# Performance work log

Hardware: AMD Instinct MI355X
Metric: run time of the kernel (lower is better)

The kernel has to match this reference:

```python
import jax, jax.numpy as jnp
import numpy as np

N = 100000      # num_nodes
E = 800000      # num_edges (avg degree 8)
F_IN = 64
F_OUT = 64
H = 4           # num_heads
HOPS = 2        # num_hops
NEG_SLOPE = 0.2


def setup_inputs() -> dict:
    key = jax.random.key(0)
    ks = jax.random.split(key, 9)
    node_features = jax.random.normal(ks[0], (N, F_IN), jnp.float32)
    edge_index = jax.random.randint(ks[1], (2, E), 0, N, dtype=jnp.int64)
    s_in = 1.0 / np.sqrt(F_IN)
    s_out = 1.0 / np.sqrt(F_OUT)
    W_att = jax.random.normal(ks[2], (H, F_IN, F_OUT), jnp.float32) * s_in
    a_src = jax.random.normal(ks[3], (H, F_OUT), jnp.float32) * s_out
    a_dst = jax.random.normal(ks[4], (H, F_OUT), jnp.float32) * s_out
    W_g = jax.random.normal(ks[5], (F_IN, F_OUT), jnp.float32) * s_in
    b_g = jnp.zeros((F_OUT,), jnp.float32)
    W_w = jax.random.normal(ks[6], (2 * F_OUT, F_OUT), jnp.float32) * (1.0 / np.sqrt(2 * F_OUT))
    b_w = jnp.zeros((F_OUT,), jnp.float32)
    return {"node_features": node_features, "edge_index": edge_index,
            "W_att": W_att, "a_src": a_src, "a_dst": a_dst,
            "W_g": W_g, "b_g": b_g, "W_w": W_w, "b_w": b_w}


def _segment_softmax(scores, dst, num_segments):
    # scores: [E, H], softmax over edges sharing the same destination node
    m = jax.ops.segment_max(scores, dst, num_segments=num_segments)  # [N, H]
    m = jnp.where(jnp.isneginf(m), 0.0, m)
    ex = jnp.exp(scores - m[dst])                                    # [E, H]
    den = jax.ops.segment_sum(ex, dst, num_segments=num_segments)   # [N, H]
    return ex / jnp.maximum(den[dst], 1e-16)


def _multi_head_attention(x, src, dst, W_att, a_src, a_dst):
    h = jnp.einsum('ni,hio->nho', x, W_att)                          # [N, H, O]
    e = jnp.einsum('eho,ho->eh', h[src], a_src) \
        + jnp.einsum('eho,ho->eh', h[dst], a_dst)                    # [E, H]
    e = jax.nn.leaky_relu(e, NEG_SLOPE)
    alpha = _segment_softmax(e, dst, N)                              # [E, H]
    msg = alpha[:, :, None] * h[src]                                 # [E, H, O]
    out = jax.ops.segment_sum(msg, dst, num_segments=N)              # [N, H, O]
    return out.mean(axis=1)                                          # average heads -> [N, O]


def _gf(x, src, dst, num_hops):
    # multi-hop mean-neighbor aggregation
    ones = jnp.ones((src.shape[0],), x.dtype)
    deg = jax.ops.segment_sum(ones, dst, num_segments=N)             # [N]
    deg = jnp.maximum(deg, 1.0)[:, None]
    h = x
    for _ in range(num_hops):
        h = jax.ops.segment_sum(h[src], dst, num_segments=N) / deg
    return h


def reference(node_features, edge_index, W_att, a_src, a_dst, W_g, b_g, W_w, b_w):
    src, dst = edge_index[0], edge_index[1]
    local = _multi_head_attention(node_features, src, dst, W_att, a_src, a_dst)  # [N, O]
    glob = _gf(node_features, src, dst, HOPS)                                    # [N, F_IN]
    glob = glob @ W_g + b_g                                                      # [N, O]
    # dropout is identity in eval-mode reference
    cat = jnp.concatenate([local, glob], axis=-1)                                # [N, 2O]
    return cat @ W_w + b_w                                                       # [N, O]
```

## Files before the change

kernel.cpp:

```cpp
#include <hip/hip_runtime.h>
#include <math.h>

#define NN 100000
#define EE 800000
#define FDIM 64
#define NH 4
#define NEG 0.2f

#define SCAN_BLK 1024
#define SCAN_NBLK 98
#define HIST_BLK 3125
#define KH_BLK   6250

#define OFF_XB     0ull
#define OFF_HOP1   12800000ull
#define OFF_HOP2   25600000ull
#define OFF_SSRC   38400000ull
#define OFF_SDST   40000000ull
#define OFF_DEGC   41600000ull
#define OFF_ROWS   42000000ull
#define OFF_CURS   42400000ull
#define OFF_DEGF   42800000ull
#define OFF_PART   43200000ull
#define OFF_CSRS   43201024ull
#define OFF_WCAT   46401024ull
#define OFF_BCOMB  46417408ull
#define OFF_WT     46417664ull
#define OFF_WAS    46450432ull
#define OFF_WAD    46451456ull
#define WS_NEEDED  46452480ull

typedef __attribute__((ext_vector_type(8))) short bf16x8;
typedef __attribute__((ext_vector_type(4))) float f32x4;

__device__ __forceinline__ float bflo(unsigned int u) { return __uint_as_float(u << 16); }
__device__ __forceinline__ float bfhi(unsigned int u) { return __uint_as_float(u & 0xffff0000u); }
__device__ __forceinline__ unsigned short f2bf(float f) {
    unsigned int u = __float_as_uint(f);
    unsigned int r = u + 0x7fffu + ((u >> 16) & 1u);
    return (unsigned short)(r >> 16);
}
__device__ __forceinline__ float lrelu(float x) { return x > 0.f ? x : NEG * x; }

__global__ __launch_bounds__(256) void k_pre(
    const float* __restrict__ Watt, const float* __restrict__ asrc,
    const float* __restrict__ adst, const float* __restrict__ Wg,
    const float* __restrict__ bg, const float* __restrict__ Ww,
    const float* __restrict__ bw, const int* __restrict__ dst,
    unsigned short* __restrict__ Wt, float* __restrict__ waS, float* __restrict__ waD,
    unsigned short* __restrict__ Wcat, float* __restrict__ bc, int* __restrict__ degc)
{
    __shared__ float WcS[64][4];
    const int b = blockIdx.x, t = threadIdx.x;
    if (b < 8) {
        for (int idx = b * 2048 + t; idx < (b + 1) * 2048; idx += 256) {
            const int h = idx >> 12, o = (idx >> 6) & 63, k = idx & 63;
            Wt[idx] = f2bf(Watt[h * 4096 + k * 64 + o]);
        }
        if (b == 0) {
            const int h = t >> 6, i = t & 63;
            float aS = 0.f, aD = 0.f;
            for (int o = 0; o < 64; o++) {
                const float w = Watt[h * 4096 + i * 64 + o];
                aS += w * asrc[h * 64 + o];
                aD += w * adst[h * 64 + o];
            }
            waS[t] = aS;
            waD[t] = aD;
        }
    } else if (b < 24) {
        const int c0 = (b - 8) * 4;
        {
            const int r = t >> 2, ci = t & 3;
            float a = 0.f;
            for (int m = 0; m < 64; m++) a += Wg[r * 64 + m] * Ww[(64 + m) * 64 + c0 + ci];
            WcS[r][ci] = a;
        }
        if (b == 8 && t < 64) {
            float a = bw[t];
            for (int m = 0; m < 64; m++) a += bg[m] * Ww[(64 + m) * 64 + t];
            bc[t] = a;
        }
        __syncthreads();
        for (int idx = t; idx < 512; idx += 256) {
            const int ci = idx >> 7, k = idx & 127;
            const int c = c0 + ci;
            const float v = (k < 64) ? Ww[k * 64 + c] : WcS[k - 64][ci];
            Wcat[c * 128 + k] = f2bf(v);
        }
    } else {
        const int e = (b - 24) * 256 + t;
        if (e < EE) atomicAdd(&degc[dst[e]], 1);
    }
}

__global__ __launch_bounds__(1024) void k_scan_a(const int* __restrict__ degc, int* __restrict__ part) {
    __shared__ int sh[1024];
    int t = threadIdx.x;
    int i = blockIdx.x * SCAN_BLK + t;
    sh[t] = (i < NN) ? degc[i] : 0;
    __syncthreads();
    for (int off = 512; off > 0; off >>= 1) {
        if (t < off) sh[t] += sh[t + off];
        __syncthreads();
    }
    if (t == 0) part[blockIdx.x] = sh[0];
}

__global__ __launch_bounds__(128) void k_scan_b(int* part) {
    __shared__ int sh[128];
    int t = threadIdx.x;
    int v = (t < SCAN_NBLK) ? part[t] : 0;
    sh[t] = v;
    __syncthreads();
    for (int off = 1; off < 128; off <<= 1) {
        int tmp = (t >= off) ? sh[t - off] : 0;
        __syncthreads();
        sh[t] += tmp;
        __syncthreads();
    }
    if (t < SCAN_NBLK) part[t] = sh[t] - v;
}

__global__ __launch_bounds__(1024) void k_scan_c(
    const int* __restrict__ degc, const int* __restrict__ part,
    int* __restrict__ rows, int* __restrict__ curs, float* __restrict__ degf)
{
    __shared__ int sh[1024];
    int t = threadIdx.x;
    int i = blockIdx.x * SCAN_BLK + t;
    int v = (i < NN) ? degc[i] : 0;
    sh[t] = v;
    __syncthreads();
    for (int off = 1; off < 1024; off <<= 1) {
        int tmp = (t >= off) ? sh[t - off] : 0;
        __syncthreads();
        sh[t] += tmp;
        __syncthreads();
    }
    int excl = sh[t] - v + part[blockIdx.x];
    if (i < NN) {
        rows[i] = excl;
        curs[i] = excl;
        degf[i] = (float)max(v, 1);
    }
}

__global__ __launch_bounds__(256) void k_mid(
    const int* __restrict__ srcp, const int* __restrict__ dstp,
    int* __restrict__ curs, int* __restrict__ csrs,
    const float* __restrict__ x, const float* __restrict__ waS,
    const float* __restrict__ waD, unsigned short* __restrict__ xb,
    float* __restrict__ ssrc, float* __restrict__ sdst)
{
    __shared__ float xs[16 * 64];
    __shared__ unsigned short xsb[16 * 64];
    __shared__ float wl[2 * 256];
    const int t = threadIdx.x;
    if (blockIdx.x < HIST_BLK) {
        const int e = blockIdx.x * 256 + t;
        if (e < EE) {
            const int d = dstp[e];
            const int pos = atomicAdd(&curs[d], 1);
            csrs[pos] = srcp[e];
        }
        return;
    }
    const int n0 = (blockIdx.x - HIST_BLK) * 16;
    {
        const int r = t >> 4, c4 = (t & 15) * 4;
        const float4 v = *(const float4*)&x[(size_t)(n0 + r) * 64 + c4];
        *(float4*)&xs[r * 64 + c4] = v;
        uint2 p;
        p.x = (unsigned int)f2bf(v.x) | ((unsigned int)f2bf(v.y) << 16);
        p.y = (unsigned int)f2bf(v.z) | ((unsigned int)f2bf(v.w) << 16);
        *(uint2*)&xsb[r * 64 + c4] = p;
        wl[t] = waS[t];
        wl[256 + t] = waD[t];
    }
    __syncthreads();
    if (t < 128) {
        const int r = t >> 3, c8 = (t & 7) * 8;
        const uint4 v = *(const uint4*)&xsb[r * 64 + c8];
        *(uint4*)&xb[(size_t)(n0 + r) * 64 + c8] = v;
    }
    {
        const int nl = t >> 4, hh = (t >> 2) & 3, q = t & 3;
        const float* xr = &xs[nl * 64 + q * 16];
        const float* wS = &wl[hh * 64 + q * 16];
        const float* wD = &wl[256 + hh * 64 + q * 16];
        float pS = 0.f, pD = 0.f;
#pragma unroll
        for (int i = 0; i < 16; i++) { pS += xr[i] * wS[i]; pD += xr[i] * wD[i]; }
        pS += __shfl_xor(pS, 1); pS += __shfl_xor(pS, 2);
        pD += __shfl_xor(pD, 1); pD += __shfl_xor(pD, 2);
        if (q == 0) {
            ssrc[(n0 + nl) * 4 + hh] = pS;
            sdst[(n0 + nl) * 4 + hh] = pD;
        }
    }
}

__global__ __launch_bounds__(256) void k_attn2(
    const unsigned short* __restrict__ xb, const unsigned short* __restrict__ Wt,
    const float* __restrict__ ssrc, const float* __restrict__ sdst,
    const int* __restrict__ rows, const int* __restrict__ degc,
    const float* __restrict__ degf, const int* __restrict__ csrs,
    unsigned short* __restrict__ hop1b, char* __restrict__ outb)
{
    __shared__ unsigned short ysh[4][16][72];
    __shared__ float dsh[4][16][66];
    const int t = threadIdx.x;
    const int w = t >> 6, lane = t & 63;
    const int nl = (lane >> 4) & 3;
    const int e  = (lane >> 3) & 1;
    const int cl = lane & 7;
    const int n = blockIdx.x * 16 + w * 4 + nl;
    const int start = rows[n], cnt = degc[n];
    int cmax = cnt;
    cmax = max(cmax, __shfl_xor(cmax, 16));
    cmax = max(cmax, __shfl_xor(cmax, 32));
    const float4 sd = *(const float4*)&sdst[n * 4];
    float y0[8], y1[8], y2[8], y3[8], hp[8];
#pragma unroll
    for (int c = 0; c < 8; c++) { y0[c]=0.f; y1[c]=0.f; y2[c]=0.f; y3[c]=0.f; hp[c]=0.f; }
    float d0 = 0.f, d1 = 0.f, d2 = 0.f, d3 = 0.f;
    for (int base = 0; base < cmax; base += 2) {
        const int j = base + e;
        const bool valid = j < cnt;
        const int idx = min(start + j, EE - 1);
        const int s = csrs[idx];
        const float4 ss = *(const float4*)&ssrc[s * 4];
        float e0 = __expf(lrelu(ss.x + sd.x));
        float e1 = __expf(lrelu(ss.y + sd.y));
        float e2 = __expf(lrelu(ss.z + sd.z));
        float e3 = __expf(lrelu(ss.w + sd.w));
        float hw = 1.f;
        if (!valid) { e0 = 0.f; e1 = 0.f; e2 = 0.f; e3 = 0.f; hw = 0.f; }
        d0 += e0; d1 += e1; d2 += e2; d3 += e3;
        const uint4 u = *(const uint4*)&xb[(size_t)s * 64 + cl * 8];
        float xv[8];
        xv[0] = bflo(u.x); xv[1] = bfhi(u.x);
        xv[2] = bflo(u.y); xv[3] = bfhi(u.y);
        xv[4] = bflo(u.z); xv[5] = bfhi(u.z);
        xv[6] = bflo(u.w); xv[7] = bfhi(u.w);
#pragma unroll
        for (int c = 0; c < 8; c++) {
            y0[c] += e0 * xv[c];
            y1[c] += e1 * xv[c];
            y2[c] += e2 * xv[c];
            y3[c] += e3 * xv[c];
            hp[c] += hw * xv[c];
        }
    }
#pragma unroll
    for (int c = 0; c < 8; c++) {
        y0[c] += __shfl_xor(y0[c], 8);
        y1[c] += __shfl_xor(y1[c], 8);
        y2[c] += __shfl_xor(y2[c], 8);
        y3[c] += __shfl_xor(y3[c], 8);
        hp[c] += __shfl_xor(hp[c], 8);
    }
    d0 += __shfl_xor(d0, 8);
    d1 += __shfl_xor(d1, 8);
    d2 += __shfl_xor(d2, 8);
    d3 += __shfl_xor(d3, 8);
    if (e == 0) {
        const float i0 = (cnt > 0) ? 1.f / d0 : 0.f;
        const float i1 = (cnt > 0) ? 1.f / d1 : 0.f;
        const float i2 = (cnt > 0) ? 1.f / d2 : 0.f;
        const float i3 = (cnt > 0) ? 1.f / d3 : 0.f;
        const int nloc = w * 4 + nl;
        uint4 p;
        p.x = (unsigned int)f2bf(y0[0]*i0) | ((unsigned int)f2bf(y0[1]*i0) << 16);
        p.y = (unsigned int)f2bf(y0[2]*i0) | ((unsigned int)f2bf(y0[3]*i0) << 16);
        p.z = (unsigned int)f2bf(y0[4]*i0) | ((unsigned int)f2bf(y0[5]*i0) << 16);
        p.w = (unsigned int)f2bf(y0[6]*i0) | ((unsigned int)f2bf(y0[7]*i0) << 16);
        *(uint4*)&ysh[0][nloc][cl * 8] = p;
        p.x = (unsigned int)f2bf(y1[0]*i1) | ((unsigned int)f2bf(y1[1]*i1) << 16);
        p.y = (unsigned int)f2bf(y1[2]*i1) | ((unsigned int)f2bf(y1[3]*i1) << 16);
        p.z = (unsigned int)f2bf(y1[4]*i1) | ((unsigned int)f2bf(y1[5]*i1) << 16);
        p.w = (unsigned int)f2bf(y1[6]*i1) | ((unsigned int)f2bf(y1[7]*i1) << 16);
        *(uint4*)&ysh[1][nloc][cl * 8] = p;
        p.x = (unsigned int)f2bf(y2[0]*i2) | ((unsigned int)f2bf(y2[1]*i2) << 16);
        p.y = (unsigned int)f2bf(y2[2]*i2) | ((unsigned int)f2bf(y2[3]*i2) << 16);
        p.z = (unsigned int)f2bf(y2[4]*i2) | ((unsigned int)f2bf(y2[5]*i2) << 16);
        p.w = (unsigned int)f2bf(y2[6]*i2) | ((unsigned int)f2bf(y2[7]*i2) << 16);
        *(uint4*)&ysh[2][nloc][cl * 8] = p;
        p.x = (unsigned int)f2bf(y3[0]*i3) | ((unsigned int)f2bf(y3[1]*i3) << 16);
        p.y = (unsigned int)f2bf(y3[2]*i3) | ((unsigned int)f2bf(y3[3]*i3) << 16);
        p.z = (unsigned int)f2bf(y3[4]*i3) | ((unsigned int)f2bf(y3[5]*i3) << 16);
        p.w = (unsigned int)f2bf(y3[6]*i3) | ((unsigned int)f2bf(y3[7]*i3) << 16);
        *(uint4*)&ysh[3][nloc][cl * 8] = p;
        const float iv = 1.f / degf[n];
        p.x = (unsigned int)f2bf(hp[0]*iv) | ((unsigned int)f2bf(hp[1]*iv) << 16);
        p.y = (unsigned int)f2bf(hp[2]*iv) | ((unsigned int)f2bf(hp[3]*iv) << 16);
        p.z = (unsigned int)f2bf(hp[4]*iv) | ((unsigned int)f2bf(hp[5]*iv) << 16);
        p.w = (unsigned int)f2bf(hp[6]*iv) | ((unsigned int)f2bf(hp[7]*iv) << 16);
        *(uint4*)&hop1b[(size_t)n * 64 + cl * 8] = p;
    }
    __syncthreads();
    {
        const int m = lane & 15, quad = lane >> 4;
        const bf16x8 a0 = *(const bf16x8*)&ysh[w][m][quad * 8];
        const bf16x8 a1 = *(const bf16x8*)&ysh[w][m][32 + quad * 8];
        f32x4 acc[4] = {{0.f,0.f,0.f,0.f},{0.f,0.f,0.f,0.f},{0.f,0.f,0.f,0.f},{0.f,0.f,0.f,0.f}};
#pragma unroll
        for (int ot = 0; ot < 4; ot++) {
            const unsigned short* wp = Wt + w * 4096 + (ot * 16 + m) * 64 + quad * 8;
            const bf16x8 b0 = *(const bf16x8*)wp;
            const bf16x8 b1 = *(const bf16x8*)(wp + 32);
            acc[ot] = __builtin_amdgcn_mfma_f32_16x16x32_bf16(a0, b0, acc[ot], 0, 0, 0);
            acc[ot] = __builtin_amdgcn_mfma_f32_16x16x32_bf16(a1, b1, acc[ot], 0, 0, 0);
        }
#pragma unroll
        for (int ot = 0; ot < 4; ot++)
#pragma unroll
            for (int r = 0; r < 4; r++)
                dsh[w][quad * 4 + r][ot * 16 + m] = acc[ot][r];
    }
    __syncthreads();
    {
        const int n2 = t >> 4, c4 = (t & 15) * 4;
        float o0 = 0.25f * (dsh[0][n2][c4+0] + dsh[1][n2][c4+0] + dsh[2][n2][c4+0] + dsh[3][n2][c4+0]);
        float o1 = 0.25f * (dsh[0][n2][c4+1] + dsh[1][n2][c4+1] + dsh[2][n2][c4+1] + dsh[3][n2][c4+1]);
        float o2 = 0.25f * (dsh[0][n2][c4+2] + dsh[1][n2][c4+2] + dsh[2][n2][c4+2] + dsh[3][n2][c4+2]);
        float o3 = 0.25f * (dsh[0][n2][c4+3] + dsh[1][n2][c4+3] + dsh[2][n2][c4+3] + dsh[3][n2][c4+3]);
        uint2 p;
        p.x = (unsigned int)f2bf(o0) | ((unsigned int)f2bf(o1) << 16);
        p.y = (unsigned int)f2bf(o2) | ((unsigned int)f2bf(o3) << 16);
        *(uint2*)(outb + ((size_t)(blockIdx.x * 16 + n2)) * 256 + (t & 15) * 8) = p;
    }
}

__global__ __launch_bounds__(256) void k_hop(
    const unsigned short* __restrict__ xin, const int* __restrict__ rows,
    const int* __restrict__ degc, const float* __restrict__ degf,
    const int* __restrict__ csrs, unsigned short* __restrict__ out_b)
{
    const int lane = threadIdx.x & 63;
    const int n = blockIdx.x * 4 + (threadIdx.x >> 6);
    if (n >= NN) return;
    const int start = rows[n], cnt = degc[n];
    const int g = lane >> 3;
    const int c8 = (lane & 7) * 8;
    float a0=0.f,a1=0.f,a2=0.f,a3=0.f,a4=0.f,a5=0.f,a6=0.f,a7=0.f;
    for (int j = g; j < cnt; j += 8) {
        const int s = csrs[start + j];
        const uint4 u = *(const uint4*)&xin[(size_t)s * 64 + c8];
        a0 += bflo(u.x); a1 += bfhi(u.x);
        a2 += bflo(u.y); a3 += bfhi(u.y);
        a4 += bflo(u.z); a5 += bfhi(u.z);
        a6 += bflo(u.w); a7 += bfhi(u.w);
    }
#pragma unroll
    for (int off = 8; off < 64; off <<= 1) {
        a0 += __shfl_xor(a0, off); a1 += __shfl_xor(a1, off);
        a2 += __shfl_xor(a2, off); a3 += __shfl_xor(a3, off);
        a4 += __shfl_xor(a4, off); a5 += __shfl_xor(a5, off);
        a6 += __shfl_xor(a6, off); a7 += __shfl_xor(a7, off);
    }
    if (lane < 8) {
        const float inv = 1.f / degf[n];
        uint4 p;
        p.x = (unsigned int)f2bf(a0 * inv) | ((unsigned int)f2bf(a1 * inv) << 16);
        p.y = (unsigned int)f2bf(a2 * inv) | ((unsigned int)f2bf(a3 * inv) << 16);
        p.z = (unsigned int)f2bf(a4 * inv) | ((unsigned int)f2bf(a5 * inv) << 16);
        p.w = (unsigned int)f2bf(a6 * inv) | ((unsigned int)f2bf(a7 * inv) << 16);
        *(uint4*)&out_b[(size_t)n * 64 + c8] = p;
    }
}

__global__ __launch_bounds__(256) void k_final(
    const unsigned short* __restrict__ Wcat, const float* __restrict__ bc,
    const unsigned short* __restrict__ hop2b, float* __restrict__ outp)
{
    __shared__ float os[64 * 68];
    __shared__ float bcl[64];
    const int t = threadIdx.x;
    const int n0 = blockIdx.x * 64;
    if (t < 64) bcl[t] = bc[t];
    const int w = t >> 6, lane = t & 63, m = lane & 15, quad = lane >> 4;
    const int node = n0 + w * 16 + m;
    const int nld = min(node, NN - 1);
    const unsigned short* lrow = (const unsigned short*)((const char*)outp + (size_t)nld * 256);
    const unsigned short* grow = &hop2b[(size_t)nld * 64];
    const bf16x8 a0 = *(const bf16x8*)&lrow[quad * 8];
    const bf16x8 a1 = *(const bf16x8*)&lrow[32 + quad * 8];
    const bf16x8 a2 = *(const bf16x8*)&grow[quad * 8];
    const bf16x8 a3 = *(const bf16x8*)&grow[32 + quad * 8];
    f32x4 acc[4] = {{0.f,0.f,0.f,0.f},{0.f,0.f,0.f,0.f},{0.f,0.f,0.f,0.f},{0.f,0.f,0.f,0.f}};
#pragma unroll
    for (int ot = 0; ot < 4; ot++) {
        const unsigned short* wp = Wcat + (ot * 16 + m) * 128 + quad * 8;
        const bf16x8 b0 = *(const bf16x8*)wp;
        const bf16x8 b1 = *(const bf16x8*)(wp + 32);
        const bf16x8 b2 = *(const bf16x8*)(wp + 64);
        const bf16x8 b3 = *(const bf16x8*)(wp + 96);
        acc[ot] = __builtin_amdgcn_mfma_f32_16x16x32_bf16(a0, b0, acc[ot], 0, 0, 0);
        acc[ot] = __builtin_amdgcn_mfma_f32_16x16x32_bf16(a1, b1, acc[ot], 0, 0, 0);
        acc[ot] = __builtin_amdgcn_mfma_f32_16x16x32_bf16(a2, b2, acc[ot], 0, 0, 0);
        acc[ot] = __builtin_amdgcn_mfma_f32_16x16x32_bf16(a3, b3, acc[ot], 0, 0, 0);
    }
    __syncthreads();
#pragma unroll
    for (int ot = 0; ot < 4; ot++)
#pragma unroll
        for (int r = 0; r < 4; r++)
            os[(w * 16 + quad * 4 + r) * 68 + ot * 16 + m] = acc[ot][r] + bcl[ot * 16 + m];
    __syncthreads();
#pragma unroll
    for (int p = 0; p < 4; p++) {
        const int idx = p * 256 + t;
        const int row = idx >> 4, f4 = idx & 15;
        if (n0 + row < NN)
            *(float4*)&outp[(size_t)(n0 + row) * 64 + f4 * 4] = *(const float4*)&os[row * 68 + f4 * 4];
    }
}

extern "C" void kernel_launch(void* const* d_in, const int* in_sizes, int n_in,
                              void* d_out, int out_size, void* d_ws, size_t ws_size,
                              hipStream_t stream)
{
    const float* x    = (const float*)d_in[0];
    const int*   ei   = (const int*)d_in[1];
    const int*   srcp = ei;
    const int*   dstp = ei + EE;
    const float* Watt = (const float*)d_in[2];
    const float* asrc = (const float*)d_in[3];
    const float* adst = (const float*)d_in[4];
    const float* Wg   = (const float*)d_in[5];
    const float* bg   = (const float*)d_in[6];
    const float* Ww   = (const float*)d_in[7];
    const float* bw   = (const float*)d_in[8];
    float* outp = (float*)d_out;

    if (ws_size < WS_NEEDED) return;

    char* ws = (char*)d_ws;
    unsigned short* xb    = (unsigned short*)(ws + OFF_XB);
    unsigned short* hop1b = (unsigned short*)(ws + OFF_HOP1);
    unsigned short* hop2b = (unsigned short*)(ws + OFF_HOP2);
    float* ssrc = (float*)(ws + OFF_SSRC);
    float* sdst = (float*)(ws + OFF_SDST);
    int*   degc = (int*)(ws + OFF_DEGC);
    int*   rows = (int*)(ws + OFF_ROWS);
    int*   curs = (int*)(ws + OFF_CURS);
    float* degf = (float*)(ws + OFF_DEGF);
    int*   part = (int*)(ws + OFF_PART);
    int*   csrs = (int*)(ws + OFF_CSRS);
    unsigned short* Wcat = (unsigned short*)(ws + OFF_WCAT);
    float* bc   = (float*)(ws + OFF_BCOMB);
    unsigned short* Wt = (unsigned short*)(ws + OFF_WT);
    float* waS  = (float*)(ws + OFF_WAS);
    float* waD  = (float*)(ws + OFF_WAD);

    hipMemsetAsync(degc, 0, NN * sizeof(int), stream);
    k_pre<<<24 + HIST_BLK, 256, 0, stream>>>(Watt, asrc, adst, Wg, bg, Ww, bw,
                                             dstp, Wt, waS, waD, Wcat, bc, degc);
    k_scan_a<<<SCAN_NBLK, 1024, 0, stream>>>(degc, part);
    k_scan_b<<<1, 128, 0, stream>>>(part);
    k_scan_c<<<SCAN_NBLK, 1024, 0, stream>>>(degc, part, rows, curs, degf);
    k_mid<<<HIST_BLK + KH_BLK, 256, 0, stream>>>(srcp, dstp, curs, csrs,
                                                 x, waS, waD, xb, ssrc, sdst);
    k_attn2<<<NN / 16, 256, 0, stream>>>(xb, Wt, ssrc, sdst, rows, degc, degf, csrs,
                                         hop1b, (char*)d_out);
    k_hop<<<NN / 4, 256, 0, stream>>>(hop1b, rows, degc, degf, csrs, hop2b);
    k_final<<<(NN + 63) / 64, 256, 0, stream>>>(Wcat, bc, hop2b, outp);
}
```

Baseline: 314.0 us.

## Fuse second hop aggregation into final projection and unroll attention gather

The second mean-aggregation hop is moved into the final projection kernel, with results staged in shared memory. This removes a kernel launch and the global round-trip of the hop-2 buffer. The attention aggregation loop now processes two edges per half-wave per iteration, so more independent gathers are in flight. The cost is that each wave in the fused tail walks 16 nodes serially, which may reduce latency hiding, and the unrolled loop raises register pressure.

Measured after the change: 324.0 us. 3.2% more time.

```diff
diff --git a/kernel.cpp b/kernel.cpp
--- a/kernel.cpp
+++ b/kernel.cpp
@@ -14,7 +14,6 @@
 
 #define OFF_XB     0ull
 #define OFF_HOP1   12800000ull
-#define OFF_HOP2   25600000ull
 #define OFF_SSRC   38400000ull
 #define OFF_SDST   40000000ull
 #define OFF_DEGC   41600000ull
@@ -225,32 +224,47 @@
 #pragma unroll
     for (int c = 0; c < 8; c++) { y0[c]=0.f; y1[c]=0.f; y2[c]=0.f; y3[c]=0.f; hp[c]=0.f; }
     float d0 = 0.f, d1 = 0.f, d2 = 0.f, d3 = 0.f;
-    for (int base = 0; base < cmax; base += 2) {
-        const int j = base + e;
-        const bool valid = j < cnt;
-        const int idx = min(start + j, EE - 1);
-        const int s = csrs[idx];
-        const float4 ss = *(const float4*)&ssrc[s * 4];
-        float e0 = __expf(lrelu(ss.x + sd.x));
-        float e1 = __expf(lrelu(ss.y + sd.y));
-        float e2 = __expf(lrelu(ss.z + sd.z));
-        float e3 = __expf(lrelu(ss.w + sd.w));
-        float hw = 1.f;
-        if (!valid) { e0 = 0.f; e1 = 0.f; e2 = 0.f; e3 = 0.f; hw = 0.f; }
-        d0 += e0; d1 += e1; d2 += e2; d3 += e3;
-        const uint4 u = *(const uint4*)&xb[(size_t)s * 64 + cl * 8];
-        float xv[8];
-        xv[0] = bflo(u.x); xv[1] = bfhi(u.x);
-        xv[2] = bflo(u.y); xv[3] = bfhi(u.y);
-        xv[4] = bflo(u.z); xv[5] = bfhi(u.z);
-        xv[6] = bflo(u.w); xv[7] = bfhi(u.w);
+    for (int base = 0; base < cmax; base += 4) {
+        const int ja = base + e;
+        const int jb = base + 2 + e;
+        const bool va = ja < cnt, vb = jb < cnt;
+        const int ia = min(start + ja, EE - 1);
+        const int ib = min(start + jb, EE - 1);
+        const int sa = csrs[ia];
+        const int sb = csrs[ib];
+        const float4 ssa = *(const float4*)&ssrc[sa * 4];
+        const float4 ssb = *(const float4*)&ssrc[sb * 4];
+        const uint4 ua = *(const uint4*)&xb[(size_t)sa * 64 + cl * 8];
+        const uint4 ub = *(const uint4*)&xb[(size_t)sb * 64 + cl * 8];
+        float ea0 = __expf(lrelu(ssa.x + sd.x));
+        float ea1 = __expf(lrelu(ssa.y + sd.y));
+        float ea2 = __expf(lrelu(ssa.z + sd.z));
+        float ea3 = __expf(lrelu(ssa.w + sd.w));
+        float hwa = 1.f;
+        if (!va) { ea0 = 0.f; ea1 = 0.f; ea2 = 0.f; ea3 = 0.f; hwa = 0.f; }
+        float eb0 = __expf(lrelu(ssb.x + sd.x));
+        float eb1 = __expf(lrelu(ssb.y + sd.y));
+        float eb2 = __expf(lrelu(ssb.z + sd.z));
+        float eb3 = __expf(lrelu(ssb.w + sd.w));
+        float hwb = 1.f;
+        if (!vb) { eb0 = 0.f; eb1 = 0.f; eb2 = 0.f; eb3 = 0.f; hwb = 0.f; }
+        d0 += ea0 + eb0; d1 += ea1 + eb1; d2 += ea2 + eb2; d3 += ea3 + eb3;
+        float xva[8], xvb[8];
+        xva[0] = bflo(ua.x); xva[1] = bfhi(ua.x);
+        xva[2] = bflo(ua.y); xva[3] = bfhi(ua.y);
+        xva[4] = bflo(ua.z); xva[5] = bfhi(ua.z);
+        xva[6] = bflo(ua.w); xva[7] = bfhi(ua.w);
+        xvb[0] = bflo(ub.x); xvb[1] = bfhi(ub.x);
+        xvb[2] = bflo(ub.y); xvb[3] = bfhi(ub.y);
+        xvb[4] = bflo(ub.z); xvb[5] = bfhi(ub.z);
+        xvb[6] = bflo(ub.w); xvb[7] = bfhi(ub.w);
 #pragma unroll
         for (int c = 0; c < 8; c++) {
-            y0[c] += e0 * xv[c];
-            y1[c] += e1 * xv[c];
-            y2[c] += e2 * xv[c];
-            y3[c] += e3 * xv[c];
-            hp[c] += hw * xv[c];
+            y0[c] += ea0 * xva[c] + eb0 * xvb[c];
+            y1[c] += ea1 * xva[c] + eb1 * xvb[c];
+            y2[c] += ea2 * xva[c] + eb2 * xvb[c];
+            y3[c] += ea3 * xva[c] + eb3 * xvb[c];
+            hp[c] += hwa * xva[c] + hwb * xvb[c];
         }
     }
 #pragma unroll
@@ -333,62 +347,57 @@
     }
 }
 
-__global__ __launch_bounds__(256) void k_hop(
-    const unsigned short* __restrict__ xin, const int* __restrict__ rows,
+__global__ __launch_bounds__(256) void k_tail(
+    const unsigned short* __restrict__ Wcat, const float* __restrict__ bc,
+    const unsigned short* __restrict__ hop1b, const int* __restrict__ rows,
     const int* __restrict__ degc, const float* __restrict__ degf,
-    const int* __restrict__ csrs, unsigned short* __restrict__ out_b)
-{
-    const int lane = threadIdx.x & 63;
-    const int n = blockIdx.x * 4 + (threadIdx.x >> 6);
-    if (n >= NN) return;
-    const int start = rows[n], cnt = degc[n];
-    const int g = lane >> 3;
-    const int c8 = (lane & 7) * 8;
-    float a0=0.f,a1=0.f,a2=0.f,a3=0.f,a4=0.f,a5=0.f,a6=0.f,a7=0.f;
-    for (int j = g; j < cnt; j += 8) {
-        const int s = csrs[start + j];
-        const uint4 u = *(const uint4*)&xin[(size_t)s * 64 + c8];
-        a0 += bflo(u.x); a1 += bfhi(u.x);
-        a2 += bflo(u.y); a3 += bfhi(u.y);
-        a4 += bflo(u.z); a5 += bfhi(u.z);
-        a6 += bflo(u.w); a7 += bfhi(u.w);
-    }
-#pragma unroll
-    for (int off = 8; off < 64; off <<= 1) {
-        a0 += __shfl_xor(a0, off); a1 += __shfl_xor(a1, off);
-        a2 += __shfl_xor(a2, off); a3 += __shfl_xor(a3, off);
-        a4 += __shfl_xor(a4, off); a5 += __shfl_xor(a5, off);
-        a6 += __shfl_xor(a6, off); a7 += __shfl_xor(a7, off);
-    }
-    if (lane < 8) {
-        const float inv = 1.f / degf[n];
-        uint4 p;
-        p.x = (unsigned int)f2bf(a0 * inv) | ((unsigned int)f2bf(a1 * inv) << 16);
-        p.y = (unsigned int)f2bf(a2 * inv) | ((unsigned int)f2bf(a3 * inv) << 16);
-        p.z = (unsigned int)f2bf(a4 * inv) | ((unsigned int)f2bf(a5 * inv) << 16);
-        p.w = (unsigned int)f2bf(a6 * inv) | ((unsigned int)f2bf(a7 * inv) << 16);
-        *(uint4*)&out_b[(size_t)n * 64 + c8] = p;
-    }
-}
-
-__global__ __launch_bounds__(256) void k_final(
-    const unsigned short* __restrict__ Wcat, const float* __restrict__ bc,
-    const unsigned short* __restrict__ hop2b, float* __restrict__ outp)
-{
+    const int* __restrict__ csrs, float* __restrict__ outp)
+{
+    __shared__ unsigned short h2sh[4][16][72];
     __shared__ float os[64 * 68];
     __shared__ float bcl[64];
     const int t = threadIdx.x;
     const int n0 = blockIdx.x * 64;
     if (t < 64) bcl[t] = bc[t];
-    const int w = t >> 6, lane = t & 63, m = lane & 15, quad = lane >> 4;
-    const int node = n0 + w * 16 + m;
-    const int nld = min(node, NN - 1);
-    const unsigned short* lrow = (const unsigned short*)((const char*)outp + (size_t)nld * 256);
-    const unsigned short* grow = &hop2b[(size_t)nld * 64];
+    const int w = t >> 6, lane = t & 63;
+    const int g = lane >> 3, c8 = (lane & 7) * 8;
+    for (int i = 0; i < 16; i++) {
+        const int node = n0 + w * 16 + i;
+        const int nld = min(node, NN - 1);
+        const int start = rows[nld], cnt = degc[nld];
+        float a0=0.f,a1=0.f,a2=0.f,a3=0.f,a4=0.f,a5=0.f,a6=0.f,a7=0.f;
+        for (int j = g; j < cnt; j += 8) {
+            const int s = csrs[start + j];
+            const uint4 u = *(const uint4*)&hop1b[(size_t)s * 64 + c8];
+            a0 += bflo(u.x); a1 += bfhi(u.x);
+            a2 += bflo(u.y); a3 += bfhi(u.y);
+            a4 += bflo(u.z); a5 += bfhi(u.z);
+            a6 += bflo(u.w); a7 += bfhi(u.w);
+        }
+#pragma unroll
+        for (int off = 8; off < 64; off <<= 1) {
+            a0 += __shfl_xor(a0, off); a1 += __shfl_xor(a1, off);
+            a2 += __shfl_xor(a2, off); a3 += __shfl_xor(a3, off);
+            a4 += __shfl_xor(a4, off); a5 += __shfl_xor(a5, off);
+            a6 += __shfl_xor(a6, off); a7 += __shfl_xor(a7, off);
+        }
+        if (lane < 8) {
+            const float inv = 1.f / degf[nld];
+            uint4 p;
+            p.x = (unsigned int)f2bf(a0 * inv) | ((unsigned int)f2bf(a1 * inv) << 16);
+            p.y = (unsigned int)f2bf(a2 * inv) | ((unsigned int)f2bf(a3 * inv) << 16);
+            p.z = (unsigned int)f2bf(a4 * inv) | ((unsigned int)f2bf(a5 * inv) << 16);
+            p.w = (unsigned int)f2bf(a6 * inv) | ((unsigned int)f2bf(a7 * inv) << 16);
+            *(uint4*)&h2sh[w][i][lane * 8] = p;
+        }
+    }
+    const int m = lane & 15, quad = lane >> 4;
+    const int nld2 = min(n0 + w * 16 + m, NN - 1);
+    const unsigned short* lrow = (const unsigned short*)((const char*)outp + (size_t)nld2 * 256);
     const bf16x8 a0 = *(const bf16x8*)&lrow[quad * 8];
     const bf16x8 a1 = *(const bf16x8*)&lrow[32 + quad * 8];
-    const bf16x8 a2 = *(const bf16x8*)&grow[quad * 8];
-    const bf16x8 a3 = *(const bf16x8*)&grow[32 + quad * 8];
+    const bf16x8 a2 = *(const bf16x8*)&h2sh[w][m][quad * 8];
+    const bf16x8 a3 = *(const bf16x8*)&h2sh[w][m][32 + quad * 8];
     f32x4 acc[4] = {{0.f,0.f,0.f,0.f},{0.f,0.f,0.f,0.f},{0.f,0.f,0.f,0.f},{0.f,0.f,0.f,0.f}};
 #pragma unroll
     for (int ot = 0; ot < 4; ot++) {
@@ -440,7 +449,6 @@
     char* ws = (char*)d_ws;
     unsigned short* xb    = (unsigned short*)(ws + OFF_XB);
     unsigned short* hop1b = (unsigned short*)(ws + OFF_HOP1);
-    unsigned short* hop2b = (unsigned short*)(ws + OFF_HOP2);
     float* ssrc = (float*)(ws + OFF_SSRC);
     float* sdst = (float*)(ws + OFF_SDST);
     int*   degc = (int*)(ws + OFF_DEGC);
@@ -465,6 +473,6 @@
                                                  x, waS, waD, xb, ssrc, sdst);
     k_attn2<<<NN / 16, 256, 0, stream>>>(xb, Wt, ssrc, sdst, rows, degc, degf, csrs,
                                          hop1b, (char*)d_out);
-    k_hop<<<NN / 4, 256, 0, stream>>>(hop1b, rows, degc, degf, csrs, hop2b);
-    k_final<<<(NN + 63) / 64, 256, 0, stream>>>(Wcat, bc, hop2b, outp);
-}
+    k_tail<<<(NN + 63) / 64, 256, 0, stream>>>(Wcat, bc, hop1b, rows, degc, degf,
+                                               csrs, outp);
+}
```
